# Optimization experiments

Hardware: AMD Instinct MI355X
Metric: run time of the kernel (lower is better)

Reference implementation:

```python
import jax, jax.numpy as jnp
import numpy as np

B, T, L, H = 8, 32, 512, 768  # batch docs, decode steps, encoder length, BART-base hidden


def setup_inputs() -> dict:
    key = jax.random.key(0)
    ks = jax.random.split(key, 7)
    sc = 1.0 / np.sqrt(H).astype(np.float32)
    return {
        "encoder_hn": jax.random.normal(ks[0], (B, L, H), jnp.float32),
        "dec": jax.random.normal(ks[1], (B, T, H), jnp.float32),   # decoder_rnn outputs per step
        "W1": jax.random.normal(ks[2], (H, H), jnp.float32) * sc,  # nnW1 (no bias)
        "W2": jax.random.normal(ks[3], (H, H), jnp.float32) * sc,  # nnW2 (no bias)
        "v": jax.random.normal(ks[4], (H,), jnp.float32) * sc,     # nnV (no bias)
        "starts": jax.random.randint(ks[5], (B, T), 0, 128, jnp.int32),  # ragged slice start per step
        "lens": jax.random.randint(ks[6], (B,), 300, L + 1, jnp.int32),  # curL per document
    }


def reference(encoder_hn, dec, W1, W2, v, starts, lens):
    # pointerLayer batched over (b, t):
    #   WE = nnW1(en)          -> [B, L, H]
    #   WD = nnW2(di expanded) -> [B, T, H]
    #   scores = selu( nnV( selu(WE + WD) ) )  over positions [start, len)
    WE = jnp.einsum('blh,kh->blk', encoder_hn, W1)                 # [B, L, H]
    WD = jnp.einsum('bth,kh->btk', dec, W2)                        # [B, T, H]
    act = jax.nn.selu(WE[:, None, :, :] + WD[:, :, None, :])      # [B, T, L, H]
    scores = jax.nn.selu(jnp.einsum('btlh,h->btl', act, v))       # [B, T, L]
    # ragged slice curencoder_hn[start:curL] expressed as a mask
    pos = jnp.arange(L, dtype=jnp.int32)
    mask = (pos[None, None, :] >= starts[:, :, None]) & \
           (pos[None, None, :] < lens[:, None, None])              # [B, T, L]
    NEG = jnp.asarray(-1e30, scores.dtype)
    logp = jax.nn.log_softmax(jnp.where(mask, scores, NEG), axis=-1)
    return jnp.where(mask, logp, jnp.zeros((), logp.dtype))       # masked log-probs [B, T, L]
```

## Files before the change

### kernel.cpp

```cpp
#include <hip/hip_runtime.h>
#include <math.h>

constexpr int Bn = 8, Tn = 32, Ln = 512, Hn = 768;

typedef __attribute__((ext_vector_type(8))) short bf16x8;
typedef __attribute__((ext_vector_type(4))) float f32x4;

__device__ __forceinline__ short f2bf(float x) {
    unsigned u = __float_as_uint(x);
    u += 0x7FFFu + ((u >> 16) & 1u);
    return (short)(u >> 16);
}
__device__ __forceinline__ float bf2f(unsigned short s) {
    return __uint_as_float(((unsigned)s) << 16);
}

constexpr float kScale = 1.0507009873554804934193349852946f;
constexpr float kAS    = 1.7580993408473768f;

__device__ __forceinline__ float selu(float x) {
    return x > 0.f ? kScale * x : fmaf(kAS, __expf(x), -kAS);
}

__global__ __launch_bounds__(256) void cvt_bf16_multi(
    const float* __restrict__ s0, short* __restrict__ d0, int c0,
    const float* __restrict__ s1, short* __restrict__ d1, int c1,
    const float* __restrict__ s2, short* __restrict__ d2, int c2,
    const float* __restrict__ s3, short* __restrict__ d3, int c3)
{
    const int i = blockIdx.x * 256 + threadIdx.x;
    if (i >= c3) return;
    const float* s; short* d; int off;
    if (i < c0)      { s = s0; d = d0; off = i; }
    else if (i < c1) { s = s1; d = d1; off = i - c0; }
    else if (i < c2) { s = s2; d = d2; off = i - c1; }
    else             { s = s3; d = d3; off = i - c2; }
    const float4 f = ((const float4*)s)[off];
    short4 r;
    r.x = f2bf(f.x); r.y = f2bf(f.y); r.z = f2bf(f.z); r.w = f2bf(f.w);
    ((short4*)d)[off] = r;
}

__global__ __launch_bounds__(256) void gemm2_bf16_nt(
    const short* __restrict__ A1, const short* __restrict__ B1,
    unsigned short* __restrict__ C1, int M1,
    const short* __restrict__ A2, const short* __restrict__ B2,
    unsigned short* __restrict__ C2,
    int N, int K)
{
    constexpr int BM = 128, BN = 128, BK = 32;
    __shared__ __align__(16) short As[BM * BK];
    __shared__ __align__(16) short Bs[BN * BK];

    const int nblk1 = M1 / BM;
    const int bx = blockIdx.x;
    const short* A; const short* Bm; unsigned short* C; int bm;
    if (bx < nblk1) { A = A1; Bm = B1; C = C1; bm = bx * BM; }
    else            { A = A2; Bm = B2; C = C2; bm = (bx - nblk1) * BM; }
    const int bn = blockIdx.y * BN;

    const int tid  = threadIdx.x;
    const int lane = tid & 63;
    const int wv   = tid >> 6;
    const int quad = lane >> 4;
    const int l16  = lane & 15;
    const int wm   = (wv & 1) * 64;
    const int wn   = (wv >> 1) * 64;

    const int sr = lane >> 2;
    const int kq = (lane & 3) << 3;

    f32x4 acc[4][4] = {};

    for (int k0 = 0; k0 < K; k0 += BK) {
        const int ra = wv * 16 + sr;
        __builtin_amdgcn_global_load_lds(
            (const __attribute__((address_space(1))) unsigned int*)(A + (size_t)(bm + ra) * K + k0 + kq),
            (__attribute__((address_space(3))) unsigned int*)(As + ra * BK + kq), 16, 0, 0);
        __builtin_amdgcn_global_load_lds(
            (const __attribute__((address_space(1))) unsigned int*)(A + (size_t)(bm + 64 + ra) * K + k0 + kq),
            (__attribute__((address_space(3))) unsigned int*)(As + (64 + ra) * BK + kq), 16, 0, 0);
        __builtin_amdgcn_global_load_lds(
            (const __attribute__((address_space(1))) unsigned int*)(Bm + (size_t)(bn + ra) * K + k0 + kq),
            (__attribute__((address_space(3))) unsigned int*)(Bs + ra * BK + kq), 16, 0, 0);
        __builtin_amdgcn_global_load_lds(
            (const __attribute__((address_space(1))) unsigned int*)(Bm + (size_t)(bn + 64 + ra) * K + k0 + kq),
            (__attribute__((address_space(3))) unsigned int*)(Bs + (64 + ra) * BK + kq), 16, 0, 0);
        __syncthreads();

        bf16x8 af[4], bfr[4];
#pragma unroll
        for (int i = 0; i < 4; ++i)
            af[i] = *(const bf16x8*)&As[(wm + i * 16 + l16) * BK + quad * 8];
#pragma unroll
        for (int j = 0; j < 4; ++j)
            bfr[j] = *(const bf16x8*)&Bs[(wn + j * 16 + l16) * BK + quad * 8];
#pragma unroll
        for (int i = 0; i < 4; ++i)
#pragma unroll
            for (int j = 0; j < 4; ++j)
                acc[i][j] = __builtin_amdgcn_mfma_f32_16x16x32_bf16(af[i], bfr[j], acc[i][j], 0, 0, 0);
        __syncthreads();
    }

#pragma unroll
    for (int i = 0; i < 4; ++i)
#pragma unroll
        for (int j = 0; j < 4; ++j)
#pragma unroll
            for (int rr = 0; rr < 4; ++rr) {
                const int row = bm + wm + i * 16 + quad * 4 + rr;
                const int col = bn + wn + j * 16 + l16;
                C[(size_t)row * N + col] = (unsigned short)f2bf(acc[i][j][rr]);
            }
}

__global__ __launch_bounds__(512) void scores_softmax_fused(
    const unsigned short* __restrict__ WE,
    const unsigned short* __restrict__ WD,
    const float* __restrict__ v,
    const int* __restrict__ starts,
    const int* __restrict__ lens,
    float* __restrict__ out)
{
    const int bid = blockIdx.x;
    const int b = bid & 7;
    const int t = bid >> 3;
    const int bt = b * Tn + t;
    const int tid = threadIdx.x;
    const int lane = tid & 63;
    const int wv = tid >> 6;

    __shared__ float sc[Ln];
    __shared__ float red[16];

    const int start = starts[bt];
    const int len = lens[b];

    float wdr[12], vr[12];
#pragma unroll
    for (int j = 0; j < 3; ++j) {
        const int h = (lane << 2) + (j << 8);
        const ushort4 wdu = *(const ushort4*)(WD + (size_t)bt * Hn + h);
        const float4 vv = *(const float4*)(v + h);
        wdr[j * 4 + 0] = bf2f(wdu.x); wdr[j * 4 + 1] = bf2f(wdu.y);
        wdr[j * 4 + 2] = bf2f(wdu.z); wdr[j * 4 + 3] = bf2f(wdu.w);
        vr[j * 4 + 0] = vv.x; vr[j * 4 + 1] = vv.y;
        vr[j * 4 + 2] = vv.z; vr[j * 4 + 3] = vv.w;
    }

    const unsigned short* WEb = WE + (size_t)b * Ln * Hn;

    for (int k = 0; k < 16; ++k) {
        const int g = wv + (k << 3);
        const int lg = g << 2;
        if (lg + 3 < start || lg >= len) continue;

        ushort4 weu[4][3];
#pragma unroll
        for (int rr = 0; rr < 4; ++rr) {
            const unsigned short* row = WEb + (size_t)(lg + rr) * Hn;
#pragma unroll
            for (int j = 0; j < 3; ++j)
                weu[rr][j] = *(const ushort4*)(row + (lane << 2) + (j << 8));
        }
        float s[4] = {0.f, 0.f, 0.f, 0.f};
#pragma unroll
        for (int j = 0; j < 3; ++j) {
#pragma unroll
            for (int rr = 0; rr < 4; ++rr) {
                float x;
                x = bf2f(weu[rr][j].x) + wdr[j * 4 + 0]; s[rr] = fmaf(selu(x), vr[j * 4 + 0], s[rr]);
                x = bf2f(weu[rr][j].y) + wdr[j * 4 + 1]; s[rr] = fmaf(selu(x), vr[j * 4 + 1], s[rr]);
                x = bf2f(weu[rr][j].z) + wdr[j * 4 + 2]; s[rr] = fmaf(selu(x), vr[j * 4 + 2], s[rr]);
                x = bf2f(weu[rr][j].w) + wdr[j * 4 + 3]; s[rr] = fmaf(selu(x), vr[j * 4 + 3], s[rr]);
            }
        }
#pragma unroll
        for (int off = 32; off > 0; off >>= 1) {
#pragma unroll
            for (int rr = 0; rr < 4; ++rr)
                s[rr] += __shfl_xor(s[rr], off, 64);
        }
        if (lane == 0) {
#pragma unroll
            for (int rr = 0; rr < 4; ++rr)
                sc[lg + rr] = selu(s[rr]);
        }
    }
    __syncthreads();

    const int l = tid;
    const bool msk = (l >= start) && (l < len);
    const float val = msk ? sc[l] : -1e30f;

    float mx = val;
#pragma unroll
    for (int off = 32; off > 0; off >>= 1)
        mx = fmaxf(mx, __shfl_xor(mx, off, 64));
    if (lane == 0) red[wv] = mx;
    __syncthreads();
    mx = red[0];
#pragma unroll
    for (int i = 1; i < 8; ++i) mx = fmaxf(mx, red[i]);

    float sm = msk ? __expf(val - mx) : 0.f;
#pragma unroll
    for (int off = 32; off > 0; off >>= 1)
        sm += __shfl_xor(sm, off, 64);
    if (lane == 0) red[8 + wv] = sm;
    __syncthreads();
    float tot = red[8];
#pragma unroll
    for (int i = 1; i < 8; ++i) tot += red[8 + i];

    const float logZ = mx + __logf(tot);
    out[(size_t)bt * Ln + l] = msk ? (val - logZ) : 0.f;
}

extern "C" void kernel_launch(void* const* d_in, const int* in_sizes, int n_in,
                              void* d_out, int out_size, void* d_ws, size_t ws_size,
                              hipStream_t stream) {
    const float* enc    = (const float*)d_in[0];
    const float* dec    = (const float*)d_in[1];
    const float* W1     = (const float*)d_in[2];
    const float* W2     = (const float*)d_in[3];
    const float* v      = (const float*)d_in[4];
    const int*   starts = (const int*)d_in[5];
    const int*   lens   = (const int*)d_in[6];
    float* out = (float*)d_out;

    constexpr int n_enc = Bn * Ln * Hn;
    constexpr int n_dec = Bn * Tn * Hn;
    constexpr int n_w   = Hn * Hn;

    const size_t need = (size_t)(n_enc + n_dec + 2 * n_w) * 2
                      + (size_t)(n_enc + n_dec) * 2;
    if (ws_size < need) return;

    short* enc16 = (short*)d_ws;
    short* dec16 = enc16 + n_enc;
    short* w1_16 = dec16 + n_dec;
    short* w2_16 = w1_16 + n_w;
    unsigned short* WE16 = (unsigned short*)(w2_16 + n_w);
    unsigned short* WD16 = WE16 + n_enc;

    constexpr int c0 = n_enc / 4;
    constexpr int c1 = c0 + n_dec / 4;
    constexpr int c2 = c1 + n_w / 4;
    constexpr int c3 = c2 + n_w / 4;
    cvt_bf16_multi<<<dim3((c3 + 255) / 256), dim3(256), 0, stream>>>(
        enc, enc16, c0, dec, dec16, c1, W1, w1_16, c2, W2, w2_16, c3);

    gemm2_bf16_nt<<<dim3((Bn * Ln) / 128 + (Bn * Tn) / 128, Hn / 128),
                    dim3(256), 0, stream>>>(
        enc16, w1_16, WE16, Bn * Ln,
        dec16, w2_16, WD16, Hn, Hn);

    scores_softmax_fused<<<dim3(Bn * Tn), dim3(512), 0, stream>>>(
        WE16, WD16, v, starts, lens, out);
}
```

Measured before the change: 129.2 us.

## Double-buffer GEMM LDS tiles and widen scores kernel to 1024 threads

The bf16 GEMM now keeps two LDS buffers for the A and B tiles. It issues the async global-to-LDS loads for the next K tile before running the MFMAs on the current one, so load latency overlaps compute and one barrier per iteration is removed. The scores/softmax kernel is launched with 1024 threads (16 waves), so each wave handles half as many 4-row groups, with guards so only the first 512 threads join the softmax and write output. The cost is doubled LDS use per GEMM block, which may lower occupancy, plus idle waves during the softmax phase.

```diff
diff --git a/kernel.cpp b/kernel.cpp
--- a/kernel.cpp
+++ b/kernel.cpp
@@ -49,8 +49,8 @@
     int N, int K)
 {
     constexpr int BM = 128, BN = 128, BK = 32;
-    __shared__ __align__(16) short As[BM * BK];
-    __shared__ __align__(16) short Bs[BN * BK];
+    __shared__ __align__(16) short As[2][BM * BK];
+    __shared__ __align__(16) short Bs[2][BN * BK];
 
     const int nblk1 = M1 / BM;
     const int bx = blockIdx.x;
@@ -69,32 +69,40 @@
 
     const int sr = lane >> 2;
     const int kq = (lane & 3) << 3;
+    const int ra = wv * 16 + sr;
 
     f32x4 acc[4][4] = {};
 
+    auto stage = [&](int buf, int k0) {
+        __builtin_amdgcn_global_load_lds(
+            (const __attribute__((address_space(1))) unsigned int*)(A + (size_t)(bm + ra) * K + k0 + kq),
+            (__attribute__((address_space(3))) unsigned int*)(&As[buf][ra * BK + kq]), 16, 0, 0);
+        __builtin_amdgcn_global_load_lds(
+            (const __attribute__((address_space(1))) unsigned int*)(A + (size_t)(bm + 64 + ra) * K + k0 + kq),
+            (__attribute__((address_space(3))) unsigned int*)(&As[buf][(64 + ra) * BK + kq]), 16, 0, 0);
+        __builtin_amdgcn_global_load_lds(
+            (const __attribute__((address_space(1))) unsigned int*)(Bm + (size_t)(bn + ra) * K + k0 + kq),
+            (__attribute__((address_space(3))) unsigned int*)(&Bs[buf][ra * BK + kq]), 16, 0, 0);
+        __builtin_amdgcn_global_load_lds(
+            (const __attribute__((address_space(1))) unsigned int*)(Bm + (size_t)(bn + 64 + ra) * K + k0 + kq),
+            (__attribute__((address_space(3))) unsigned int*)(&Bs[buf][(64 + ra) * BK + kq]), 16, 0, 0);
+    };
+
+    stage(0, 0);
+    __syncthreads();
+
     for (int k0 = 0; k0 < K; k0 += BK) {
-        const int ra = wv * 16 + sr;
-        __builtin_amdgcn_global_load_lds(
-            (const __attribute__((address_space(1))) unsigned int*)(A + (size_t)(bm + ra) * K + k0 + kq),
-            (__attribute__((address_space(3))) unsigned int*)(As + ra * BK + kq), 16, 0, 0);
-        __builtin_amdgcn_global_load_lds(
-            (const __attribute__((address_space(1))) unsigned int*)(A + (size_t)(bm + 64 + ra) * K + k0 + kq),
-            (__attribute__((address_space(3))) unsigned int*)(As + (64 + ra) * BK + kq), 16, 0, 0);
-        __builtin_amdgcn_global_load_lds(
-            (const __attribute__((address_space(1))) unsigned int*)(Bm + (size_t)(bn + ra) * K + k0 + kq),
-            (__attribute__((address_space(3))) unsigned int*)(Bs + ra * BK + kq), 16, 0, 0);
-        __builtin_amdgcn_global_load_lds(
-            (const __attribute__((address_space(1))) unsigned int*)(Bm + (size_t)(bn + 64 + ra) * K + k0 + kq),
-            (__attribute__((address_space(3))) unsigned int*)(Bs + (64 + ra) * BK + kq), 16, 0, 0);
-        __syncthreads();
+        const int cur = (k0 / BK) & 1;
+        const int nxt = cur ^ 1;
+        if (k0 + BK < K) stage(nxt, k0 + BK);
 
         bf16x8 af[4], bfr[4];
 #pragma unroll
         for (int i = 0; i < 4; ++i)
-            af[i] = *(const bf16x8*)&As[(wm + i * 16 + l16) * BK + quad * 8];
+            af[i] = *(const bf16x8*)&As[cur][(wm + i * 16 + l16) * BK + quad * 8];
 #pragma unroll
         for (int j = 0; j < 4; ++j)
-            bfr[j] = *(const bf16x8*)&Bs[(wn + j * 16 + l16) * BK + quad * 8];
+            bfr[j] = *(const bf16x8*)&Bs[cur][(wn + j * 16 + l16) * BK + quad * 8];
 #pragma unroll
         for (int i = 0; i < 4; ++i)
 #pragma unroll
@@ -115,7 +123,7 @@
             }
 }
 
-__global__ __launch_bounds__(512) void scores_softmax_fused(
+__global__ __launch_bounds__(1024) void scores_softmax_fused(
     const unsigned short* __restrict__ WE,
     const unsigned short* __restrict__ WD,
     const float* __restrict__ v,
@@ -151,8 +159,8 @@
 
     const unsigned short* WEb = WE + (size_t)b * Ln * Hn;
 
-    for (int k = 0; k < 16; ++k) {
-        const int g = wv + (k << 3);
+    for (int k = 0; k < 8; ++k) {
+        const int g = wv + (k << 4);
         const int lg = g << 2;
         if (lg + 3 < start || lg >= len) continue;
 
@@ -191,14 +199,15 @@
     __syncthreads();
 
     const int l = tid;
-    const bool msk = (l >= start) && (l < len);
+    const bool active = (l < Ln);
+    const bool msk = active && (l >= start) && (l < len);
     const float val = msk ? sc[l] : -1e30f;
 
     float mx = val;
 #pragma unroll
     for (int off = 32; off > 0; off >>= 1)
         mx = fmaxf(mx, __shfl_xor(mx, off, 64));
-    if (lane == 0) red[wv] = mx;
+    if (lane == 0 && wv < 8) red[wv] = mx;
     __syncthreads();
     mx = red[0];
 #pragma unroll
@@ -208,14 +217,16 @@
 #pragma unroll
     for (int off = 32; off > 0; off >>= 1)
         sm += __shfl_xor(sm, off, 64);
-    if (lane == 0) red[8 + wv] = sm;
+    if (lane == 0 && wv < 8) red[8 + wv] = sm;
     __syncthreads();
     float tot = red[8];
 #pragma unroll
     for (int i = 1; i < 8; ++i) tot += red[8 + i];
 
-    const float logZ = mx + __logf(tot);
-    out[(size_t)bt * Ln + l] = msk ? (val - logZ) : 0.f;
+    if (active) {
+        const float logZ = mx + __logf(tot);
+        out[(size_t)bt * Ln + l] = msk ? (val - logZ) : 0.f;
+    }
 }
 
 extern "C" void kernel_launch(void* const* d_in, const int* in_sizes, int n_in,
@@ -257,6 +268,6 @@
         enc16, w1_16, WE16, Bn * Ln,
         dec16, w2_16, WD16, Hn, Hn);
 
-    scores_softmax_fused<<<dim3(Bn * Tn), dim3(512), 0, stream>>>(
+    scores_softmax_fused<<<dim3(Bn * Tn), dim3(1024), 0, stream>>>(
         WE16, WD16, v, starts, lens, out);
 }
```

After: 125.5 us. 2.9% less time.
